# Performance work log

Measured on AMD Instinct MI355X. Metric: run time of the kernel, lower is better.

## Reference

```python
import jax, jax.numpy as jnp
import numpy as np

B, C, H, W = 32, 3, 512, 512


def _make_rot(N):
    k = np.arange(N, dtype=np.float64)[None, :] * np.pi / (2 * N)
    return jnp.asarray(np.cos(k), jnp.float32), jnp.asarray(np.sin(k), jnp.float32)


def setup_inputs() -> dict:
    key = jax.random.key(0)
    X = jax.random.normal(key, (B, C, H, W), dtype=jnp.float32)
    W_r_weight, W_i_weight = _make_rot(W)
    W_r_height, W_i_height = _make_rot(H)
    return {
        "X": X,
        "W_r_weight": W_r_weight,
        "W_i_weight": W_i_weight,
        "W_r_height": W_r_height,
        "W_i_height": W_i_height,
    }


def _idct1(X, W_r, W_i):
    # 1D IDCT (DCT-III) along last axis via irfft, norm='ortho'.
    shp = X.shape
    N = shp[-1]
    Xv = X.reshape(-1, N) * 0.5
    # ortho scaling: col 0 -> *sqrt(N)*2, cols 1: -> *sqrt(N/2)*2 (after the /2)
    col_scale = np.full((N,), np.sqrt(N / 2) * 2, dtype=np.float32)
    col_scale[0] = np.sqrt(N) * 2
    Xv = Xv * jnp.asarray(col_scale)
    # V_t_i[:, 0] = 0; V_t_i[:, j] = -Xv[:, N-j] for j >= 1
    Vti = jnp.concatenate([jnp.zeros_like(Xv[:, :1]), -Xv[:, :0:-1]], axis=1)
    Vr = Xv * W_r - Vti * W_i
    Vi = Xv * W_i + Vti * W_r
    v = jnp.fft.irfft(jax.lax.complex(Vr, Vi), n=N, axis=1)  # [M, N] real
    # de-interleave: even outputs from front half, odd outputs from reversed tail
    x = jnp.zeros_like(v)
    x = x.at[:, ::2].set(v[:, : N - N // 2])
    x = x.at[:, 1::2].set(v[:, ::-1][:, : N // 2])
    return x.reshape(shp)


def reference(X, W_r_weight, W_i_weight, W_r_height, W_i_height):
    x = _idct1(X, W_r_weight, W_i_weight)          # IDCT over width
    x = jnp.swapaxes(x, -1, -2)
    x = _idct1(x, W_r_height, W_i_height)          # IDCT over height
    return jnp.swapaxes(x, -1, -2)
```

## Files before the change

### kernel.cpp

```cpp
#include <hip/hip_runtime.h>
#include <math.h>
#include <stdint.h>

#define N512 512

typedef __attribute__((ext_vector_type(8))) short short8;
typedef __attribute__((ext_vector_type(4))) float floatx4;

__device__ __forceinline__ short f2bf(float f) {
    uint32_t u = __float_as_uint(f);
    uint32_t r = u + 0x7fffu + ((u >> 16) & 1u);
    return (short)(r >> 16);
}

__device__ __forceinline__ short f2bf_fast(float f) {
    return (short)((__float_as_uint(f) + 0x8000u) >> 16);
}

__device__ __forceinline__ void gload_lds16(const void* g, void* l) {
    __builtin_amdgcn_global_load_lds(
        (const __attribute__((address_space(1))) void*)g,
        (__attribute__((address_space(3))) void*)l,
        16, 0, 0);
}

__global__ __launch_bounds__(256) void build_idct_matrix_bf16(short* __restrict__ M) {
    int idx = blockIdx.x * 256 + threadIdx.x;
    int n = idx >> 9;
    int k = idx & 511;
    int j = (k * (2 * n + 1)) & (4 * N512 - 1);
    float theta = (float)j * (3.14159265358979323846f / (2.0f * (float)N512));
    float s = (k == 0) ? 0.044194173824159216f : 0.0625f;
    M[idx] = f2bf(s * cosf(theta));
}

__global__ __launch_bounds__(256) void gemm_s1(const short* __restrict__ A,
                                               const float* __restrict__ Xg,
                                               short* __restrict__ Tg) {
    __shared__ short lds[2 * 8192];
    short* ldsA = lds;
    short* ldsB = lds + 8192;

    const int t = threadIdx.x;
    const int w = t >> 6;
    const int l = t & 63;
    const int q = (t >> 4) & 3;
    const int r = t & 15;

    const int bm0 = blockIdx.y * 128;
    const int bn0 = blockIdx.x * 128;
    const int wm0 = (w >> 1) * 64;
    const int wn0 = (w & 1) * 64;

    const float* Xs = Xg + ((long)blockIdx.z << 18);
    short* Tt = Tg + ((long)blockIdx.z << 18);

    const int rsub = l >> 3;
    const int glog = (l & 7) ^ rsub;

    const int brow = t >> 4;
    const int col4 = t & 15;
    const int bg   = col4 >> 1;
    const int bh   = col4 & 1;

    floatx4 acc[4][4] = {};

    for (int kt = 0; kt < 8; ++kt) {
        const int k0 = kt * 64;
#pragma unroll
        for (int i = 0; i < 4; ++i) {
            const int chunk = w * 4 + i;
            const int rt = chunk * 8 + rsub;
            gload_lds16(A + (((long)(bm0 + rt)) << 9) + k0 + glog * 8,
                        ldsA + chunk * 512);
        }
        {
            float4 v[8];
#pragma unroll
            for (int p = 0; p < 8; ++p) {
                const int rt = p * 16 + brow;
                v[p] = *(const float4*)(Xs + (((long)(bn0 + rt)) << 9) + k0 + col4 * 4);
            }
#pragma unroll
            for (int p = 0; p < 8; ++p) {
                const int rt = p * 16 + brow;
                const int bchunk = rt >> 3;
                const int brs = rt & 7;
                short4 o;
                o.x = f2bf_fast(v[p].x);
                o.y = f2bf_fast(v[p].y);
                o.z = f2bf_fast(v[p].z);
                o.w = f2bf_fast(v[p].w);
                *(short4*)(ldsB + bchunk * 512 + brs * 64 + ((bg ^ brs) * 8) + bh * 4) = o;
            }
        }
        __syncthreads();
#pragma unroll
        for (int kk = 0; kk < 2; ++kk) {
            const int c = kk * 4 + q;
            const int goff = ((c ^ (r & 7)) * 8);
            short8 af[4], bf[4];
#pragma unroll
            for (int i = 0; i < 4; ++i) {
                af[i] = *(const short8*)(ldsA + (wm0 + i * 16 + r) * 64 + goff);
                bf[i] = *(const short8*)(ldsB + (wn0 + i * 16 + r) * 64 + goff);
            }
#pragma unroll
            for (int i = 0; i < 4; ++i)
#pragma unroll
                for (int j = 0; j < 4; ++j)
                    acc[i][j] = __builtin_amdgcn_mfma_f32_16x16x32_bf16(
                        af[i], bf[j], acc[i][j], 0, 0, 0);
        }
        __syncthreads();
    }

#pragma unroll
    for (int i = 0; i < 4; ++i) {
        const int mrow = bm0 + wm0 + i * 16 + q * 4;
#pragma unroll
        for (int j = 0; j < 4; ++j) {
            const int ncol = bn0 + wn0 + j * 16 + r;
#pragma unroll
            for (int rg = 0; rg < 4; ++rg)
                Tt[(long)(mrow + rg) * N512 + ncol] = f2bf(acc[i][j][rg]);
        }
    }
}

__global__ __launch_bounds__(256) void gemm_s2(const short* __restrict__ A,
                                               const short* __restrict__ Bg,
                                               float* __restrict__ Cg) {
    __shared__ short lds[2 * 8192];
    short* ldsA = lds;
    short* ldsB = lds + 8192;

    const int t = threadIdx.x;
    const int w = t >> 6;
    const int l = t & 63;
    const int q = (t >> 4) & 3;
    const int r = t & 15;

    const int bm0 = blockIdx.y * 128;
    const int bn0 = blockIdx.x * 128;
    const int wm0 = (w >> 1) * 64;
    const int wn0 = (w & 1) * 64;

    const short* Bs = Bg + ((long)blockIdx.z << 18);
    float* C = Cg + ((long)blockIdx.z << 18);

    const int rsub = l >> 3;
    const int glog = (l & 7) ^ rsub;

    floatx4 acc[4][4] = {};

    for (int kt = 0; kt < 8; ++kt) {
        const int k0 = kt * 64;
#pragma unroll
        for (int i = 0; i < 4; ++i) {
            const int chunk = w * 4 + i;
            const int rt = chunk * 8 + rsub;
            gload_lds16(A + (((long)(bm0 + rt)) << 9) + k0 + glog * 8,
                        ldsA + chunk * 512);
            gload_lds16(Bs + (((long)(bn0 + rt)) << 9) + k0 + glog * 8,
                        ldsB + chunk * 512);
        }
        __syncthreads();
#pragma unroll
        for (int kk = 0; kk < 2; ++kk) {
            const int c = kk * 4 + q;
            const int goff = ((c ^ (r & 7)) * 8);
            short8 af[4], bf[4];
#pragma unroll
            for (int i = 0; i < 4; ++i) {
                af[i] = *(const short8*)(ldsA + (wm0 + i * 16 + r) * 64 + goff);
                bf[i] = *(const short8*)(ldsB + (wn0 + i * 16 + r) * 64 + goff);
            }
#pragma unroll
            for (int i = 0; i < 4; ++i)
#pragma unroll
                for (int j = 0; j < 4; ++j)
                    acc[i][j] = __builtin_amdgcn_mfma_f32_16x16x32_bf16(
                        af[i], bf[j], acc[i][j], 0, 0, 0);
        }
        __syncthreads();
    }

#pragma unroll
    for (int i = 0; i < 4; ++i) {
        const int mrow = bm0 + wm0 + i * 16 + q * 4;
#pragma unroll
        for (int j = 0; j < 4; ++j) {
            const int ncol = bn0 + wn0 + j * 16 + r;
#pragma unroll
            for (int rg = 0; rg < 4; ++rg)
                C[(long)(mrow + rg) * N512 + ncol] = acc[i][j][rg];
        }
    }
}

extern "C" void kernel_launch(void* const* d_in, const int* in_sizes, int n_in,
                              void* d_out, int out_size, void* d_ws, size_t ws_size,
                              hipStream_t stream) {
    const float* X = (const float*)d_in[0];
    float* out = (float*)d_out;

    const long plane = (long)N512 * N512;
    const int slices = in_sizes[0] / (int)plane;

    short* Mb = (short*)d_ws;
    short* Tt = Mb + plane;

    long avail = (long)ws_size - plane * 2;
    int chunk = (int)(avail / (plane * 2));
    if (chunk > slices) chunk = slices;
    if (chunk < 1) chunk = 1;

    build_idct_matrix_bf16<<<dim3((int)(plane / 256)), dim3(256), 0, stream>>>(Mb);

    for (int s0 = 0; s0 < slices; s0 += chunk) {
        int c = (s0 + chunk <= slices) ? chunk : (slices - s0);
        gemm_s1<<<dim3(4, 4, c), dim3(256), 0, stream>>>(
            Mb, X + (long)s0 * plane, Tt);
        gemm_s2<<<dim3(4, 4, c), dim3(256), 0, stream>>>(
            Mb, Tt, out + (long)s0 * plane);
    }
}
```

Baseline: 237.9 us.

## Fuse matrix build and both IDCT GEMM stages into one cooperative persistent kernel

Merges the three launches (cosine matrix build, stage-1 GEMM, stage-2 GEMM) into a single cooperative kernel that uses grid.sync between phases and loops persistent blocks over tiles. It also remaps stage-1 tile order with a swizzle for odd/even chunk counts. The intent is to remove launch overhead and inter-kernel gaps. In exchange, grid size is capped at resident occupancy, and grid-wide barriers can leave blocks idle when the tile count does not divide evenly across them. The matrix is still rebuilt on every call.

After: 428.0 us. 79.9% more time.

```diff
diff --git a/kernel.cpp b/kernel.cpp
--- a/kernel.cpp
+++ b/kernel.cpp
@@ -1,6 +1,9 @@
 #include <hip/hip_runtime.h>
+#include <hip/hip_cooperative_groups.h>
 #include <math.h>
 #include <stdint.h>
+
+namespace cg = cooperative_groups;
 
 #define N512 512
 
@@ -24,20 +27,21 @@
         16, 0, 0);
 }
 
-__global__ __launch_bounds__(256) void build_idct_matrix_bf16(short* __restrict__ M) {
-    int idx = blockIdx.x * 256 + threadIdx.x;
-    int n = idx >> 9;
-    int k = idx & 511;
-    int j = (k * (2 * n + 1)) & (4 * N512 - 1);
-    float theta = (float)j * (3.14159265358979323846f / (2.0f * (float)N512));
-    float s = (k == 0) ? 0.044194173824159216f : 0.0625f;
-    M[idx] = f2bf(s * cosf(theta));
-}
-
-__global__ __launch_bounds__(256) void gemm_s1(const short* __restrict__ A,
-                                               const float* __restrict__ Xg,
-                                               short* __restrict__ Tg) {
-    __shared__ short lds[2 * 8192];
+__device__ __forceinline__ void decode_swz(int L, int c,
+                                           int& bx, int& by, int& bz) {
+    if (c & 1) {
+        bx = L & 3; by = (L >> 2) & 3; bz = L >> 4;
+    } else {
+        const int g = L >> 5, s = L & 31;
+        const int u = (g << 3) | (s & 7);
+        by = s >> 3; bx = u & 3; bz = u >> 2;
+    }
+}
+
+__device__ __forceinline__ void s1_tile(short* lds, const short* __restrict__ A,
+                                        const float* __restrict__ Xg,
+                                        short* __restrict__ Tg,
+                                        int tile, int c) {
     short* ldsA = lds;
     short* ldsB = lds + 8192;
 
@@ -47,13 +51,15 @@
     const int q = (t >> 4) & 3;
     const int r = t & 15;
 
-    const int bm0 = blockIdx.y * 128;
-    const int bn0 = blockIdx.x * 128;
+    int bx, by, bz;
+    decode_swz(tile, c, bx, by, bz);
+    const int bm0 = by * 128;
+    const int bn0 = bx * 128;
     const int wm0 = (w >> 1) * 64;
     const int wn0 = (w & 1) * 64;
 
-    const float* Xs = Xg + ((long)blockIdx.z << 18);
-    short* Tt = Tg + ((long)blockIdx.z << 18);
+    const float* Xs = Xg + ((long)bz << 18);
+    short* Tt = Tg + ((long)bz << 18);
 
     const int rsub = l >> 3;
     const int glog = (l & 7) ^ rsub;
@@ -69,48 +75,46 @@
         const int k0 = kt * 64;
 #pragma unroll
         for (int i = 0; i < 4; ++i) {
-            const int chunk = w * 4 + i;
-            const int rt = chunk * 8 + rsub;
+            const int ch = w * 4 + i;
+            const int rt = ch * 8 + rsub;
             gload_lds16(A + (((long)(bm0 + rt)) << 9) + k0 + glog * 8,
-                        ldsA + chunk * 512);
-        }
-        {
-            float4 v[8];
-#pragma unroll
-            for (int p = 0; p < 8; ++p) {
-                const int rt = p * 16 + brow;
-                v[p] = *(const float4*)(Xs + (((long)(bn0 + rt)) << 9) + k0 + col4 * 4);
-            }
-#pragma unroll
-            for (int p = 0; p < 8; ++p) {
-                const int rt = p * 16 + brow;
-                const int bchunk = rt >> 3;
-                const int brs = rt & 7;
-                short4 o;
-                o.x = f2bf_fast(v[p].x);
-                o.y = f2bf_fast(v[p].y);
-                o.z = f2bf_fast(v[p].z);
-                o.w = f2bf_fast(v[p].w);
-                *(short4*)(ldsB + bchunk * 512 + brs * 64 + ((bg ^ brs) * 8) + bh * 4) = o;
-            }
+                        ldsA + ch * 512);
+        }
+        float4 v[8];
+#pragma unroll
+        for (int p = 0; p < 8; ++p) {
+            const int rt = p * 16 + brow;
+            v[p] = *(const float4*)(Xs + (((long)(bn0 + rt)) << 9) + k0 + col4 * 4);
+        }
+#pragma unroll
+        for (int p = 0; p < 8; ++p) {
+            const int rt = p * 16 + brow;
+            const int bch = rt >> 3;
+            const int brs = rt & 7;
+            short4 o;
+            o.x = f2bf_fast(v[p].x);
+            o.y = f2bf_fast(v[p].y);
+            o.z = f2bf_fast(v[p].z);
+            o.w = f2bf_fast(v[p].w);
+            *(short4*)(ldsB + bch * 512 + brs * 64 + ((bg ^ brs) * 8) + bh * 4) = o;
         }
         __syncthreads();
 #pragma unroll
         for (int kk = 0; kk < 2; ++kk) {
-            const int c = kk * 4 + q;
-            const int goff = ((c ^ (r & 7)) * 8);
-            short8 af[4], bf[4];
+            const int cc = kk * 4 + q;
+            const int goff = ((cc ^ (r & 7)) * 8);
+            short8 af[4], bfr[4];
 #pragma unroll
             for (int i = 0; i < 4; ++i) {
-                af[i] = *(const short8*)(ldsA + (wm0 + i * 16 + r) * 64 + goff);
-                bf[i] = *(const short8*)(ldsB + (wn0 + i * 16 + r) * 64 + goff);
+                af[i]  = *(const short8*)(ldsA + (wm0 + i * 16 + r) * 64 + goff);
+                bfr[i] = *(const short8*)(ldsB + (wn0 + i * 16 + r) * 64 + goff);
             }
 #pragma unroll
             for (int i = 0; i < 4; ++i)
 #pragma unroll
                 for (int j = 0; j < 4; ++j)
                     acc[i][j] = __builtin_amdgcn_mfma_f32_16x16x32_bf16(
-                        af[i], bf[j], acc[i][j], 0, 0, 0);
+                        af[i], bfr[j], acc[i][j], 0, 0, 0);
         }
         __syncthreads();
     }
@@ -128,10 +132,10 @@
     }
 }
 
-__global__ __launch_bounds__(256) void gemm_s2(const short* __restrict__ A,
-                                               const short* __restrict__ Bg,
-                                               float* __restrict__ Cg) {
-    __shared__ short lds[2 * 8192];
+__device__ __forceinline__ void s2_tile(short* lds, const short* __restrict__ A,
+                                        const short* __restrict__ Bg,
+                                        float* __restrict__ Cg,
+                                        int tile, int c) {
     short* ldsA = lds;
     short* ldsB = lds + 8192;
 
@@ -141,13 +145,16 @@
     const int q = (t >> 4) & 3;
     const int r = t & 15;
 
-    const int bm0 = blockIdx.y * 128;
-    const int bn0 = blockIdx.x * 128;
+    const int bx = tile & 3;
+    const int by = (tile >> 2) & 3;
+    const int bz = tile >> 4;
+    const int bm0 = by * 128;
+    const int bn0 = bx * 128;
     const int wm0 = (w >> 1) * 64;
     const int wn0 = (w & 1) * 64;
 
-    const short* Bs = Bg + ((long)blockIdx.z << 18);
-    float* C = Cg + ((long)blockIdx.z << 18);
+    const short* Bs = Bg + ((long)bz << 18);
+    float* C = Cg + ((long)bz << 18);
 
     const int rsub = l >> 3;
     const int glog = (l & 7) ^ rsub;
@@ -158,30 +165,30 @@
         const int k0 = kt * 64;
 #pragma unroll
         for (int i = 0; i < 4; ++i) {
-            const int chunk = w * 4 + i;
-            const int rt = chunk * 8 + rsub;
+            const int ch = w * 4 + i;
+            const int rt = ch * 8 + rsub;
             gload_lds16(A + (((long)(bm0 + rt)) << 9) + k0 + glog * 8,
-                        ldsA + chunk * 512);
+                        ldsA + ch * 512);
             gload_lds16(Bs + (((long)(bn0 + rt)) << 9) + k0 + glog * 8,
-                        ldsB + chunk * 512);
+                        ldsB + ch * 512);
         }
         __syncthreads();
 #pragma unroll
         for (int kk = 0; kk < 2; ++kk) {
-            const int c = kk * 4 + q;
-            const int goff = ((c ^ (r & 7)) * 8);
-            short8 af[4], bf[4];
+            const int cc = kk * 4 + q;
+            const int goff = ((cc ^ (r & 7)) * 8);
+            short8 af[4], bfr[4];
 #pragma unroll
             for (int i = 0; i < 4; ++i) {
-                af[i] = *(const short8*)(ldsA + (wm0 + i * 16 + r) * 64 + goff);
-                bf[i] = *(const short8*)(ldsB + (wn0 + i * 16 + r) * 64 + goff);
+                af[i]  = *(const short8*)(ldsA + (wm0 + i * 16 + r) * 64 + goff);
+                bfr[i] = *(const short8*)(ldsB + (wn0 + i * 16 + r) * 64 + goff);
             }
 #pragma unroll
             for (int i = 0; i < 4; ++i)
 #pragma unroll
                 for (int j = 0; j < 4; ++j)
                     acc[i][j] = __builtin_amdgcn_mfma_f32_16x16x32_bf16(
-                        af[i], bf[j], acc[i][j], 0, 0, 0);
+                        af[i], bfr[j], acc[i][j], 0, 0, 0);
         }
         __syncthreads();
     }
@@ -197,6 +204,41 @@
                 C[(long)(mrow + rg) * N512 + ncol] = acc[i][j][rg];
         }
     }
+}
+
+__global__ __launch_bounds__(256) void idct_fused(short* __restrict__ Mb,
+                                                  const float* __restrict__ X,
+                                                  short* __restrict__ Tt,
+                                                  float* __restrict__ out,
+                                                  int c) {
+    __shared__ __align__(16) short lds[2 * 8192];
+    cg::grid_group grid = cg::this_grid();
+    const int nb = (int)gridDim.x;
+    const int bid = (int)blockIdx.x;
+    const int t = (int)threadIdx.x;
+
+    for (int idx = bid * 256 + t; idx < N512 * N512; idx += nb * 256) {
+        int n = idx >> 9;
+        int k = idx & 511;
+        int j = (k * (2 * n + 1)) & (4 * N512 - 1);
+        float theta = (float)j * (3.14159265358979323846f / (2.0f * (float)N512));
+        float s = (k == 0) ? 0.044194173824159216f : 0.0625f;
+        Mb[idx] = f2bf(s * cosf(theta));
+    }
+    __threadfence();
+    grid.sync();
+    __threadfence();
+
+    const int ntile = 16 * c;
+    for (int tile = bid; tile < ntile; tile += nb)
+        s1_tile(lds, Mb, X, Tt, tile, c);
+
+    __threadfence();
+    grid.sync();
+    __threadfence();
+
+    for (int tile = bid; tile < ntile; tile += nb)
+        s2_tile(lds, Mb, Tt, out, tile, c);
 }
 
 extern "C" void kernel_launch(void* const* d_in, const int* in_sizes, int n_in,
@@ -216,13 +258,32 @@
     if (chunk > slices) chunk = slices;
     if (chunk < 1) chunk = 1;
 
-    build_idct_matrix_bf16<<<dim3((int)(plane / 256)), dim3(256), 0, stream>>>(Mb);
+    static int s_blocks = 0;
+    if (s_blocks == 0) {
+        int nbpcu = 0;
+        if (hipOccupancyMaxActiveBlocksPerMultiprocessor(
+                &nbpcu, idct_fused, 256, 0) != hipSuccess || nbpcu < 1)
+            nbpcu = 2;
+        hipDeviceProp_t prop;
+        int dev = 0;
+        int ncu = 256;
+        if (hipGetDevice(&dev) == hipSuccess &&
+            hipGetDeviceProperties(&prop, dev) == hipSuccess)
+            ncu = prop.multiProcessorCount;
+        long g = (long)nbpcu * ncu;
+        if (g > 1536) g = 1536;
+        if (g < 64) g = 64;
+        s_blocks = (int)g;
+    }
 
     for (int s0 = 0; s0 < slices; s0 += chunk) {
         int c = (s0 + chunk <= slices) ? chunk : (slices - s0);
-        gemm_s1<<<dim3(4, 4, c), dim3(256), 0, stream>>>(
-            Mb, X + (long)s0 * plane, Tt);
-        gemm_s2<<<dim3(4, 4, c), dim3(256), 0, stream>>>(
-            Mb, Tt, out + (long)s0 * plane);
-    }
-}
+        int g = s_blocks;
+        if (g > 16 * c) g = 16 * c;
+        const float* Xp = X + (long)s0 * plane;
+        float* op = out + (long)s0 * plane;
+        void* args[] = {(void*)&Mb, (void*)&Xp, (void*)&Tt, (void*)&op, (void*)&c};
+        hipLaunchCooperativeKernel((void*)idct_fused, dim3(g), dim3(256),
+                                   args, 0, stream);
+    }
+}
```

## Retile IDCT GEMMs to full 512-row M tiles with 64-wide N strips

Applied to the files above, without the earlier changes.

Both GEMM stages now give each block the whole 512-row basis matrix (M) against a 64-column strip of the input, with each wave computing 128x64 instead of 64x64. This lets each slice's X (or intermediate) strip be read exactly once rather than re-read by the four M-tile blocks, which cuts global traffic for the activation operand. In exchange the block loads the full basis matrix every k-step (72KB of LDS, more accumulators), which lowers occupancy and raises register pressure. It also reduces the grid from 16 to 8 blocks per slice.

Result: slower. 280.0 us (+17.7%).

```diff
diff --git a/kernel.cpp b/kernel.cpp
--- a/kernel.cpp
+++ b/kernel.cpp
@@ -37,23 +37,19 @@
 __global__ __launch_bounds__(256) void gemm_s1(const short* __restrict__ A,
                                                const float* __restrict__ Xg,
                                                short* __restrict__ Tg) {
-    __shared__ short lds[2 * 8192];
+    __shared__ __align__(16) short lds[36864];
     short* ldsA = lds;
-    short* ldsB = lds + 8192;
+    short* ldsB = lds + 32768;
 
     const int t = threadIdx.x;
     const int w = t >> 6;
     const int l = t & 63;
-    const int q = (t >> 4) & 3;
-    const int r = t & 15;
-
-    const int bm0 = blockIdx.y * 128;
-    const int bn0 = blockIdx.x * 128;
-    const int wm0 = (w >> 1) * 64;
-    const int wn0 = (w & 1) * 64;
-
-    const float* Xs = Xg + ((long)blockIdx.z << 18);
-    short* Tt = Tg + ((long)blockIdx.z << 18);
+    const int q = (l >> 4) & 3;
+    const int r = l & 15;
+
+    const int h0 = blockIdx.x * 64;
+    const float* Xs = Xg + ((long)blockIdx.y << 18);
+    short* Tt = Tg + ((long)blockIdx.y << 18);
 
     const int rsub = l >> 3;
     const int glog = (l & 7) ^ rsub;
@@ -63,67 +59,64 @@
     const int bg   = col4 >> 1;
     const int bh   = col4 & 1;
 
-    floatx4 acc[4][4] = {};
+    const int wm0 = w * 128;
+
+    floatx4 acc[8][4] = {};
 
     for (int kt = 0; kt < 8; ++kt) {
         const int k0 = kt * 64;
 #pragma unroll
-        for (int i = 0; i < 4; ++i) {
-            const int chunk = w * 4 + i;
-            const int rt = chunk * 8 + rsub;
-            gload_lds16(A + (((long)(bm0 + rt)) << 9) + k0 + glog * 8,
-                        ldsA + chunk * 512);
-        }
-        {
-            float4 v[8];
-#pragma unroll
-            for (int p = 0; p < 8; ++p) {
-                const int rt = p * 16 + brow;
-                v[p] = *(const float4*)(Xs + (((long)(bn0 + rt)) << 9) + k0 + col4 * 4);
+        for (int i = 0; i < 16; ++i) {
+            const int ch = w * 16 + i;
+            gload_lds16(A + (((long)(ch * 8 + rsub)) << 9) + k0 + glog * 8,
+                        ldsA + ch * 512);
+        }
+        float4 v[4];
+#pragma unroll
+        for (int p = 0; p < 4; ++p) {
+            const int rt = p * 16 + brow;
+            v[p] = *(const float4*)(Xs + (((long)(h0 + rt)) << 9) + k0 + col4 * 4);
+        }
+#pragma unroll
+        for (int p = 0; p < 4; ++p) {
+            const int rt = p * 16 + brow;
+            short4 o;
+            o.x = f2bf_fast(v[p].x);
+            o.y = f2bf_fast(v[p].y);
+            o.z = f2bf_fast(v[p].z);
+            o.w = f2bf_fast(v[p].w);
+            *(short4*)(ldsB + rt * 64 + ((bg ^ (rt & 7)) * 8) + bh * 4) = o;
+        }
+        __syncthreads();
+#pragma unroll
+        for (int kk = 0; kk < 2; ++kk) {
+            const int cc = kk * 4 + q;
+            const int goff = ((cc ^ (r & 7)) * 8);
+            short8 bfr[4];
+#pragma unroll
+            for (int nf = 0; nf < 4; ++nf)
+                bfr[nf] = *(const short8*)(ldsB + (nf * 16 + r) * 64 + goff);
+#pragma unroll
+            for (int mf = 0; mf < 8; ++mf) {
+                short8 af = *(const short8*)(ldsA + (wm0 + mf * 16 + r) * 64 + goff);
+#pragma unroll
+                for (int nf = 0; nf < 4; ++nf)
+                    acc[mf][nf] = __builtin_amdgcn_mfma_f32_16x16x32_bf16(
+                        af, bfr[nf], acc[mf][nf], 0, 0, 0);
             }
-#pragma unroll
-            for (int p = 0; p < 8; ++p) {
-                const int rt = p * 16 + brow;
-                const int bchunk = rt >> 3;
-                const int brs = rt & 7;
-                short4 o;
-                o.x = f2bf_fast(v[p].x);
-                o.y = f2bf_fast(v[p].y);
-                o.z = f2bf_fast(v[p].z);
-                o.w = f2bf_fast(v[p].w);
-                *(short4*)(ldsB + bchunk * 512 + brs * 64 + ((bg ^ brs) * 8) + bh * 4) = o;
-            }
-        }
-        __syncthreads();
-#pragma unroll
-        for (int kk = 0; kk < 2; ++kk) {
-            const int c = kk * 4 + q;
-            const int goff = ((c ^ (r & 7)) * 8);
-            short8 af[4], bf[4];
-#pragma unroll
-            for (int i = 0; i < 4; ++i) {
-                af[i] = *(const short8*)(ldsA + (wm0 + i * 16 + r) * 64 + goff);
-                bf[i] = *(const short8*)(ldsB + (wn0 + i * 16 + r) * 64 + goff);
-            }
-#pragma unroll
-            for (int i = 0; i < 4; ++i)
-#pragma unroll
-                for (int j = 0; j < 4; ++j)
-                    acc[i][j] = __builtin_amdgcn_mfma_f32_16x16x32_bf16(
-                        af[i], bf[j], acc[i][j], 0, 0, 0);
-        }
-        __syncthreads();
-    }
-
-#pragma unroll
-    for (int i = 0; i < 4; ++i) {
-        const int mrow = bm0 + wm0 + i * 16 + q * 4;
-#pragma unroll
-        for (int j = 0; j < 4; ++j) {
-            const int ncol = bn0 + wn0 + j * 16 + r;
+        }
+        __syncthreads();
+    }
+
+#pragma unroll
+    for (int mf = 0; mf < 8; ++mf) {
+        const int nrow = wm0 + mf * 16 + q * 4;
+#pragma unroll
+        for (int nf = 0; nf < 4; ++nf) {
+            const int hcol = h0 + nf * 16 + r;
 #pragma unroll
             for (int rg = 0; rg < 4; ++rg)
-                Tt[(long)(mrow + rg) * N512 + ncol] = f2bf(acc[i][j][rg]);
+                Tt[(long)(nrow + rg) * N512 + hcol] = f2bf(acc[mf][nf][rg]);
         }
     }
 }
@@ -131,70 +124,71 @@
 __global__ __launch_bounds__(256) void gemm_s2(const short* __restrict__ A,
                                                const short* __restrict__ Bg,
                                                float* __restrict__ Cg) {
-    __shared__ short lds[2 * 8192];
+    __shared__ __align__(16) short lds[36864];
     short* ldsA = lds;
-    short* ldsB = lds + 8192;
+    short* ldsB = lds + 32768;
 
     const int t = threadIdx.x;
     const int w = t >> 6;
     const int l = t & 63;
-    const int q = (t >> 4) & 3;
-    const int r = t & 15;
-
-    const int bm0 = blockIdx.y * 128;
-    const int bn0 = blockIdx.x * 128;
-    const int wm0 = (w >> 1) * 64;
-    const int wn0 = (w & 1) * 64;
-
-    const short* Bs = Bg + ((long)blockIdx.z << 18);
-    float* C = Cg + ((long)blockIdx.z << 18);
+    const int q = (l >> 4) & 3;
+    const int r = l & 15;
+
+    const int n0 = blockIdx.x * 64;
+    const short* Bs = Bg + ((long)blockIdx.y << 18);
+    float* C = Cg + ((long)blockIdx.y << 18);
 
     const int rsub = l >> 3;
     const int glog = (l & 7) ^ rsub;
 
-    floatx4 acc[4][4] = {};
+    const int wm0 = w * 128;
+
+    floatx4 acc[8][4] = {};
 
     for (int kt = 0; kt < 8; ++kt) {
         const int k0 = kt * 64;
 #pragma unroll
-        for (int i = 0; i < 4; ++i) {
-            const int chunk = w * 4 + i;
-            const int rt = chunk * 8 + rsub;
-            gload_lds16(A + (((long)(bm0 + rt)) << 9) + k0 + glog * 8,
-                        ldsA + chunk * 512);
-            gload_lds16(Bs + (((long)(bn0 + rt)) << 9) + k0 + glog * 8,
-                        ldsB + chunk * 512);
+        for (int i = 0; i < 16; ++i) {
+            const int ch = w * 16 + i;
+            gload_lds16(A + (((long)(ch * 8 + rsub)) << 9) + k0 + glog * 8,
+                        ldsA + ch * 512);
+        }
+#pragma unroll
+        for (int i = 0; i < 2; ++i) {
+            const int ch = w * 2 + i;
+            gload_lds16(Bs + (((long)(n0 + ch * 8 + rsub)) << 9) + k0 + glog * 8,
+                        ldsB + ch * 512);
         }
         __syncthreads();
 #pragma unroll
         for (int kk = 0; kk < 2; ++kk) {
-            const int c = kk * 4 + q;
-            const int goff = ((c ^ (r & 7)) * 8);
-            short8 af[4], bf[4];
-#pragma unroll
-            for (int i = 0; i < 4; ++i) {
-                af[i] = *(const short8*)(ldsA + (wm0 + i * 16 + r) * 64 + goff);
-                bf[i] = *(const short8*)(ldsB + (wn0 + i * 16 + r) * 64 + goff);
+            const int cc = kk * 4 + q;
+            const int goff = ((cc ^ (r & 7)) * 8);
+            short8 bfr[4];
+#pragma unroll
+            for (int nf = 0; nf < 4; ++nf)
+                bfr[nf] = *(const short8*)(ldsB + (nf * 16 + r) * 64 + goff);
+#pragma unroll
+            for (int mf = 0; mf < 8; ++mf) {
+                short8 af = *(const short8*)(ldsA + (wm0 + mf * 16 + r) * 64 + goff);
+#pragma unroll
+                for (int nf = 0; nf < 4; ++nf)
+                    acc[mf][nf] = __builtin_amdgcn_mfma_f32_16x16x32_bf16(
+                        af, bfr[nf], acc[mf][nf], 0, 0, 0);
             }
-#pragma unroll
-            for (int i = 0; i < 4; ++i)
-#pragma unroll
-                for (int j = 0; j < 4; ++j)
-                    acc[i][j] = __builtin_amdgcn_mfma_f32_16x16x32_bf16(
-                        af[i], bf[j], acc[i][j], 0, 0, 0);
-        }
-        __syncthreads();
-    }
-
-#pragma unroll
-    for (int i = 0; i < 4; ++i) {
-        const int mrow = bm0 + wm0 + i * 16 + q * 4;
-#pragma unroll
-        for (int j = 0; j < 4; ++j) {
-            const int ncol = bn0 + wn0 + j * 16 + r;
+        }
+        __syncthreads();
+    }
+
+#pragma unroll
+    for (int mf = 0; mf < 8; ++mf) {
+        const int mrow = wm0 + mf * 16 + q * 4;
+#pragma unroll
+        for (int nf = 0; nf < 4; ++nf) {
+            const int ncol = n0 + nf * 16 + r;
 #pragma unroll
             for (int rg = 0; rg < 4; ++rg)
-                C[(long)(mrow + rg) * N512 + ncol] = acc[i][j][rg];
+                C[(long)(mrow + rg) * N512 + ncol] = acc[mf][nf][rg];
         }
     }
 }
@@ -220,9 +214,9 @@
 
     for (int s0 = 0; s0 < slices; s0 += chunk) {
         int c = (s0 + chunk <= slices) ? chunk : (slices - s0);
-        gemm_s1<<<dim3(4, 4, c), dim3(256), 0, stream>>>(
+        gemm_s1<<<dim3(8, c), dim3(256), 0, stream>>>(
             Mb, X + (long)s0 * plane, Tt);
-        gemm_s2<<<dim3(4, 4, c), dim3(256), 0, stream>>>(
+        gemm_s2<<<dim3(8, c), dim3(256), 0, stream>>>(
             Mb, Tt, out + (long)s0 * plane);
     }
 }
```
